# Performance work log

Hardware: AMD Instinct MI355X
Metric: run time of the kernel (lower is better)

## Reference

```python
import jax, jax.numpy as jnp
import numpy as np

C_M = 256
C = 32
N_HEAD = 8
EPS = 1e-5

def setup_inputs() -> dict:
    key = jax.random.key(0)
    ks = jax.random.split(key, 8)
    S, R = 512, 384  # N_seq, N_res
    msa = jax.random.normal(ks[0], (S, R, C_M), dtype=jnp.float32)
    init = lambda k, shape: 0.02 * jax.random.normal(k, shape, dtype=jnp.float32)
    return {
        "msa": msa,
        "ln_w": jnp.ones((N_HEAD, C_M), jnp.float32),
        "ln_b": jnp.zeros((N_HEAD, C_M), jnp.float32),
        "Wq": init(ks[1], (N_HEAD, C, C_M)),
        "Wk": init(ks[2], (N_HEAD, C, C_M)),
        "Wv": init(ks[3], (N_HEAD, C, C_M)),
        "Wg": init(ks[4], (N_HEAD, C, C_M)),
        "out_W": init(ks[5], (C_M, C * N_HEAD)),
        "out_b": jnp.zeros((C_M,), jnp.float32),
    }

def reference(msa, ln_w, ln_b, Wq, Wk, Wv, Wg, out_W, out_b):
    # msa: [s, r, c_m] -> x: [r, s, c_m]; attention over the sequence axis per column
    x = jnp.transpose(msa, (1, 0, 2))
    scale = 1.0 / np.sqrt(C)
    outs = []
    for h in range(N_HEAD):  # fixed small head loop (each head has its own LayerNorm)
        mu = jnp.mean(x, axis=-1, keepdims=True)
        var = jnp.mean((x - mu) ** 2, axis=-1, keepdims=True)
        p = (x - mu) * jax.lax.rsqrt(var + EPS) * ln_w[h] + ln_b[h]  # [r, s, c_m]
        q = jnp.einsum('rsm,cm->rsc', p, Wq[h])
        k = jnp.einsum('rsm,cm->rsc', p, Wk[h])
        v = jnp.einsum('rsm,cm->rsc', p, Wv[h])
        g = jax.nn.sigmoid(jnp.einsum('rsm,cm->rsc', p, Wg[h]))
        logits = scale * jnp.einsum('rsc,rtc->rst', q, k)  # [r, s, s]
        a = jax.nn.softmax(logits, axis=-2)  # faithful: softmax over dim=-2 as in source
        o = g * jnp.einsum('rst,rtc->rsc', a, v)  # gated per-head output
        outs.append(o)
    cat = jnp.concatenate(outs, axis=2)  # [r, s, c*N_head]
    out = jnp.einsum('rsd,md->rsm', cat, out_W) + out_b
    return jnp.transpose(out, (1, 0, 2))  # back to [s, r, c_m]
```

## Files before the change

### kernel.cpp

```cpp
#include <hip/hip_runtime.h>
#include <hip/hip_bf16.h>


#define S_DIM 512
#define R_DIM 384
#define CM    256
#define NH    8
#define NROWS (S_DIM*R_DIM)

typedef unsigned short u16;
typedef unsigned int   u32;
typedef short bf16x8 __attribute__((ext_vector_type(8)));
typedef float f32x4  __attribute__((ext_vector_type(4)));
typedef float f32x16 __attribute__((ext_vector_type(16)));
typedef int   v2i    __attribute__((ext_vector_type(2)));

#define MFMA16(a,b,c) __builtin_amdgcn_mfma_f32_16x16x32_bf16((a),(b),(c),0,0,0)
#define MFMA32(a,b,c) __builtin_amdgcn_mfma_f32_32x32x16_bf16((a),(b),(c),0,0,0)

__device__ __forceinline__ float lo16f(u32 u){ return __uint_as_float(u << 16); }
__device__ __forceinline__ float hi16f(u32 u){ return __uint_as_float(u & 0xffff0000u); }
__device__ __forceinline__ float b2f(u16 x){ return __uint_as_float(((u32)x) << 16); }
__device__ __forceinline__ u16 f2bf(float f){
  u32 u = __float_as_uint(f);
  return (u16)((u + 0x7fffu + ((u >> 16) & 1u)) >> 16);
}
__device__ __forceinline__ u32 pk2(float a, float b){
  return (u32)f2bf(a) | ((u32)f2bf(b) << 16);
}
__device__ __forceinline__ u32 cvtpk(float a, float b){
  u32 d;
  asm("v_cvt_pk_bf16_f32 %0, %1, %2" : "=v"(d) : "v"(a), "v"(b));
  return d;
}
__device__ __forceinline__ v2i pl32swap(u32 a, u32 b){
  return __builtin_amdgcn_permlane32_swap((int)a, (int)b, false, false);
}
__device__ __forceinline__ f32x16 zero16(){
  f32x16 z;
  #pragma unroll
  for(int q=0;q<16;q++) z[q]=0.f;
  return z;
}

#define SC2 0.2550348653f

__global__ void prep_w(const float* __restrict__ lnw, const float* __restrict__ lnb,
                       const float* __restrict__ Wq, const float* __restrict__ Wk,
                       const float* __restrict__ Wv, const float* __restrict__ Wg,
                       const float* __restrict__ oW,
                       float* __restrict__ ball, u16* __restrict__ Wfrag,
                       u16* __restrict__ oWhi, u16* __restrict__ oWlo){
  int blk = blockIdx.x, t = threadIdx.x;
  if (blk < 1024){
    int h = blk >> 7, row = blk & 127, mat = row >> 5, c = row & 31;
    const float* Ws = (mat==0?Wq: mat==1?Wk: mat==2?Wv:Wg) + (size_t)(h*32+c)*CM;
    float4 w4 = ((const float4*)Ws)[t];
    float4 l4 = ((const float4*)(lnw + (size_t)h*CM))[t];
    float4 b4 = ((const float4*)(lnb + (size_t)h*CM))[t];
    int kc = t >> 2, gg = (t >> 1) & 1, e0 = (t & 1) * 4;
    u16* dst = Wfrag + ((size_t)(((blk>>5)*16 + kc))*64 + gg*32 + c)*8 + e0;
    *(uint2*)dst = make_uint2(pk2(w4.x*l4.x, w4.y*l4.y), pk2(w4.z*l4.z, w4.w*l4.w));
    float p = w4.x*b4.x + w4.y*b4.y + w4.z*b4.z + w4.w*b4.w;
    #pragma unroll
    for(int off=32; off; off>>=1) p += __shfl_down(p, off);
    if(t==0) ball[blk] = p;
  } else {
    int m = blk - 1024;
    float4 w4 = ((const float4*)(oW + (size_t)m*CM))[t];
    u16 h0=f2bf(w4.x), h1=f2bf(w4.y), h2=f2bf(w4.z), h3=f2bf(w4.w);
    u16 l0=f2bf(w4.x-b2f(h0)), l1=f2bf(w4.y-b2f(h1));
    u16 l2=f2bf(w4.z-b2f(h2)), l3=f2bf(w4.w-b2f(h3));
    ((uint2*)(oWhi + (size_t)m*CM))[t] = make_uint2((u32)h0|((u32)h1<<16), (u32)h2|((u32)h3<<16));
    ((uint2*)(oWlo + (size_t)m*CM))[t] = make_uint2((u32)l0|((u32)l1<<16), (u32)l2|((u32)l3<<16));
  }
}

__global__ __launch_bounds__(256) void ln_xhat(const float* __restrict__ msa,
                                               u16* __restrict__ xhat){
  const int tid = threadIdx.x;
  const int n0 = blockIdx.x*64;
  const int i = tid >> 2, p = tid & 3;
  const int n = n0 + i, rr = n >> 9, s = n & 511;
  const float* src = msa + ((size_t)s*R_DIM + rr)*CM + p*64;
  float x[64]; float sum=0.f, sq=0.f;
  #pragma unroll
  for(int j=0;j<64;j+=4){
    float4 v = *(const float4*)(src + j);
    x[j]=v.x; x[j+1]=v.y; x[j+2]=v.z; x[j+3]=v.w;
    sum += v.x+v.y+v.z+v.w;
    sq  += v.x*v.x + v.y*v.y + v.z*v.z + v.w*v.w;
  }
  sum += __shfl_xor(sum,1); sum += __shfl_xor(sum,2);
  sq  += __shfl_xor(sq,1);  sq  += __shfl_xor(sq,2);
  float mu = sum*(1.f/256.f);
  float rs = rsqrtf(sq*(1.f/256.f) - mu*mu + 1e-5f);
  u16* dst = xhat + (size_t)n*CM + p*64;
  #pragma unroll
  for(int j=0;j<64;j+=2)
    *(u32*)(dst + j) = pk2((x[j]-mu)*rs, (x[j+1]-mu)*rs);
}

#define KF    0
#define VF    32768
#define DRED  65536
#define ATTN_LDS 81920

__global__ __launch_bounds__(512,2) void attn_fused4(const u16* __restrict__ xhat,
      const u16* __restrict__ Wfrag, const float* __restrict__ ball,
      u16* __restrict__ obuf){
  extern __shared__ char sm[];
  const int bid = blockIdx.x;
  const int xcd = bid & 7, kk2 = bid >> 3;
  const int r = xcd*48 + (kk2 >> 3);
  const int head = kk2 & 7;
  const int tid  = threadIdx.x;
  const int w    = tid >> 6;
  const int lane = tid & 63;
  const int gg = lane >> 5, j = lane & 31;
  const int n0 = r * 512;

  bf16x8 Qfr[2][2];

  {
    #pragma unroll
    for(int mat=0; mat<4; mat++){
      bf16x8 Wf[16];
      const u16* wsrc = Wfrag + ((size_t)((head*4+mat)*16)*64 + lane)*8;
      #pragma unroll
      for(int kc=0;kc<16;kc++) Wf[kc] = *(const bf16x8*)(wsrc + (size_t)kc*512);
      float bias16[16]; float biasv = 0.f;
      if (mat == 2) biasv = ball[head*128 + 64 + j];
      else {
        #pragma unroll
        for(int reg=0;reg<16;reg++)
          bias16[reg] = ball[head*128 + mat*32 + (reg&3) + 8*(reg>>2) + 4*gg];
      }
      #pragma unroll
      for(int st=0; st<2; st++){
        const int stg = 2*w + st;
        const u16* xr = xhat + ((size_t)(n0 + stg*32 + j))*CM + gg*8;
        f32x16 D = zero16();
        if (mat == 2){
          #pragma unroll
          for(int kc=0;kc<16;kc++) D = MFMA32(*(const bf16x8*)(xr + kc*16), Wf[kc], D);
        } else {
          #pragma unroll
          for(int kc=0;kc<16;kc++) D = MFMA32(Wf[kc], *(const bf16x8*)(xr + kc*16), D);
        }
        if (mat == 3){
          u32 gw[8];
          #pragma unroll
          for(int p=0;p<4;p++)
            #pragma unroll
            for(int hh=0;hh<2;hh++){
              float a = D[4*p+2*hh]   + bias16[4*p+2*hh];
              float b = D[4*p+2*hh+1] + bias16[4*p+2*hh+1];
              gw[p*2+hh] = cvtpk(1.f/(1.f + __expf(-a)), 1.f/(1.f + __expf(-b)));
            }
          int srow = n0 + stg*32 + j;
          u32* ob32 = (u32*)(obuf + (size_t)srow*CM + head*32);
          #pragma unroll
          for(int p=0;p<4;p++)
            #pragma unroll
            for(int hh=0;hh<2;hh++)
              ob32[4*p + 2*gg + hh] = gw[p*2+hh];
        } else {
          if (mat == 2){
            #pragma unroll
            for(int q=0;q<16;q++) D[q] += biasv;
          } else {
            #pragma unroll
            for(int q=0;q<16;q++) D[q] += bias16[q];
          }
          u32 Wd[8];
          #pragma unroll
          for(int p=0;p<4;p++)
            #pragma unroll
            for(int hh=0;hh<2;hh++)
              Wd[p*2+hh] = cvtpk(D[4*p+2*hh], D[4*p+2*hh+1]);
          u32 frag[2][4];
          #pragma unroll
          for(int T=0;T<2;T++)
            #pragma unroll
            for(int hh=0;hh<2;hh++){
              v2i res = pl32swap(Wd[4*T+hh], Wd[4*T+2+hh]);
              frag[T][hh] = (u32)res[0]; frag[T][2+hh] = (u32)res[1];
            }
          if (mat == 0){
            #pragma unroll
            for(int T=0;T<2;T++){
              union { u32 wu[4]; bf16x8 v; } u;
              u.wu[0]=frag[T][0]; u.wu[1]=frag[T][1]; u.wu[2]=frag[T][2]; u.wu[3]=frag[T][3];
              Qfr[st][T] = u.v;
            }
          } else {
            char* outbase = sm + (mat==1? KF : VF);
            #pragma unroll
            for(int T=0;T<2;T++)
              *(uint4*)(outbase + ((size_t)(stg*2+T)*64 + lane)*16) =
                  make_uint4(frag[T][0],frag[T][1],frag[T][2],frag[T][3]);
          }
        }
      }
    }
  }
  __syncthreads();

  {
    float* dred = (float*)(sm + DRED);
    for(int tt=0; tt<16; tt++){
      bf16x8 Kt0 = *(const bf16x8*)(sm + KF + ((size_t)(tt*2+0)*64 + lane)*16);
      bf16x8 Kt1 = *(const bf16x8*)(sm + KF + ((size_t)(tt*2+1)*64 + lane)*16);
      float dp = 0.f;
      #pragma unroll
      for(int sb=0; sb<2; sb++){
        f32x16 D1 = zero16();
        D1 = MFMA32(Qfr[sb][0], Kt0, D1);
        D1 = MFMA32(Qfr[sb][1], Kt1, D1);
        #pragma unroll
        for(int q=0;q<16;q++) dp += exp2f(D1[q]*SC2);
      }
      v2i rr = pl32swap(__float_as_uint(dp), __float_as_uint(dp));
      float tot = __uint_as_float((u32)rr[0]) + __uint_as_float((u32)rr[1]);
      if (lane < 32) dred[w*512 + tt*32 + j] = tot;
    }
  }
  __syncthreads();
  {
    float* dred = (float*)(sm + DRED);
    float s = 0.f;
    #pragma unroll
    for(int ww=0; ww<8; ww++) s += dred[ww*512 + tid];
    dred[tid] = 1.f / s;
  }
  __syncthreads();

  {
    const float* ivd = (const float*)(sm + DRED);
    #pragma unroll
    for(int it=0; it<4; it++){
      int ch = tid + it*512;
      int t0 = (ch>>7)*32 + ((ch>>6)&1)*16 + ((ch>>5)&1)*8;
      u32* pw = (u32*)(sm + VF + (size_t)ch*16);
      uint4 v = *(uint4*)pw;
      u32 wv[4] = {v.x, v.y, v.z, v.w};
      u32 nw[4];
      #pragma unroll
      for(int rr2=0;rr2<4;rr2++){
        float lo = lo16f(wv[rr2]) * ivd[t0 + 2*rr2];
        float hi = hi16f(wv[rr2]) * ivd[t0 + 2*rr2 + 1];
        nw[rr2] = cvtpk(lo, hi);
      }
      *(uint4*)pw = make_uint4(nw[0],nw[1],nw[2],nw[3]);
    }
  }
  __syncthreads();

  #pragma unroll
  for(int sb=0; sb<2; sb++){
    f32x16 O = zero16();
    for(int tt=0; tt<16; tt++){
      bf16x8 Kt0 = *(const bf16x8*)(sm + KF + ((size_t)(tt*2+0)*64 + lane)*16);
      bf16x8 Kt1 = *(const bf16x8*)(sm + KF + ((size_t)(tt*2+1)*64 + lane)*16);
      bf16x8 Vt0 = *(const bf16x8*)(sm + VF + ((size_t)(tt*2+0)*64 + lane)*16);
      bf16x8 Vt1 = *(const bf16x8*)(sm + VF + ((size_t)(tt*2+1)*64 + lane)*16);
      f32x16 D = zero16();
      D = MFMA32(Kt0, Qfr[sb][0], D);
      D = MFMA32(Kt1, Qfr[sb][1], D);
      u32 Wd[8];
      #pragma unroll
      for(int p=0;p<4;p++)
        #pragma unroll
        for(int hh=0;hh<2;hh++)
          Wd[p*2+hh] = cvtpk(exp2f(D[4*p+2*hh]*SC2), exp2f(D[4*p+2*hh+1]*SC2));
      union { u32 wu[4]; bf16x8 v; } pf0, pf1;
      #pragma unroll
      for(int hh=0;hh<2;hh++){
        v2i res = pl32swap(Wd[0+hh], Wd[2+hh]);
        pf0.wu[hh] = (u32)res[0]; pf0.wu[2+hh] = (u32)res[1];
        v2i res2 = pl32swap(Wd[4+hh], Wd[6+hh]);
        pf1.wu[hh] = (u32)res2[0]; pf1.wu[2+hh] = (u32)res2[1];
      }
      O = MFMA32(Vt0, pf0.v, O);
      O = MFMA32(Vt1, pf1.v, O);
    }
    const int stg = 2*w + sb;
    const int srow = n0 + stg*32 + j;
    u32* ob32 = (u32*)(obuf + (size_t)srow*CM + head*32);
    #pragma unroll
    for(int p=0;p<4;p++)
      #pragma unroll
      for(int hh=0;hh<2;hh++){
        u32 gv = ob32[4*p + 2*gg + hh];
        float o0 = O[4*p+2*hh]   * lo16f(gv);
        float o1 = O[4*p+2*hh+1] * hi16f(gv);
        ob32[4*p + 2*gg + hh] = cvtpk(o0, o1);
      }
  }
}

__global__ __launch_bounds__(256,2) void outproj(const u16* __restrict__ obuf,
      const u16* __restrict__ oWhi, const u16* __restrict__ oWlo,
      const float* __restrict__ ob, float* __restrict__ out){
  const int tid = threadIdx.x, w = tid>>6, lane = tid&63, g = lane>>4, i = lane&15;
  const int n0 = blockIdx.x*64 + w*16;
  const char* ab = (const char*)(obuf + (size_t)(n0 + i)*CM);
  const f32x4 zf = {0.f,0.f,0.f,0.f};
  f32x4 acc[16];
  #pragma unroll
  for(int ct=0;ct<16;ct++) acc[ct] = zf;
  #pragma unroll
  for(int kk=0; kk<8; kk++){
    bf16x8 a = *(const bf16x8*)(ab + kk*64 + g*16);
    #pragma unroll
    for(int ct=0; ct<16; ct++){
      const char* wh = (const char*)(oWhi + (size_t)(ct*16 + i)*CM);
      const char* wl = (const char*)(oWlo + (size_t)(ct*16 + i)*CM);
      bf16x8 bh = *(const bf16x8*)(wh + kk*64 + g*16);
      bf16x8 bl = *(const bf16x8*)(wl + kk*64 + g*16);
      acc[ct] = MFMA16(a, bh, acc[ct]);
      acc[ct] = MFMA16(a, bl, acc[ct]);
    }
  }
  #pragma unroll
  for(int ct=0; ct<16; ct++){
    float bias = ob[ct*16 + i];
    #pragma unroll
    for(int q=0; q<4; q++){
      int n = n0 + 4*g + q;
      out[((size_t)(n & 511)*R_DIM + (n >> 9))*CM + ct*16 + i] = acc[ct][q] + bias;
    }
  }
}

extern "C" void kernel_launch(void* const* d_in, const int* in_sizes, int n_in,
                              void* d_out, int out_size, void* d_ws, size_t ws_size,
                              hipStream_t stream){
  const float* msa = (const float*)d_in[0];
  const float* lnw = (const float*)d_in[1];
  const float* lnb = (const float*)d_in[2];
  const float* Wq  = (const float*)d_in[3];
  const float* Wk  = (const float*)d_in[4];
  const float* Wv  = (const float*)d_in[5];
  const float* Wg  = (const float*)d_in[6];
  const float* oW  = (const float*)d_in[7];
  const float* ob  = (const float*)d_in[8];
  float* out = (float*)d_out;

  char* ws = (char*)d_ws;
  u16*   Wfrag  = (u16*)(ws);
  float* ball   = (float*)(ws + 524288);
  u16*   oWhi   = (u16*)(ws + 528384);
  u16*   oWlo   = (u16*)(ws + 659456);
  u16*   xhat   = (u16*)(ws + 790528);
  u16*   obuf   = (u16*)(ws + 101453824);

  (void)hipFuncSetAttribute((const void*)attn_fused4,
                      hipFuncAttributeMaxDynamicSharedMemorySize, ATTN_LDS);

  prep_w<<<dim3(1280), dim3(64), 0, stream>>>(lnw, lnb, Wq, Wk, Wv, Wg, oW,
                                              ball, Wfrag, oWhi, oWlo);
  ln_xhat<<<dim3(NROWS/64), dim3(256), 0, stream>>>(msa, xhat);
  attn_fused4<<<dim3(R_DIM*NH), dim3(512), ATTN_LDS, stream>>>(xhat, Wfrag, ball, obuf);
  outproj<<<dim3(NROWS/64), dim3(256), 0, stream>>>(obuf, oWhi, oWlo, ob, out);
}
```

Baseline: 1.139 ms.

## Rewrite output projection with 32x32 MFMA and pre-fragmented weight layout

The output projection kernel now uses 32x32x16 MFMA tiles with 32 rows per wave and 128 rows per block, and loops over output column tiles instead of keeping all sixteen 16-wide accumulators live. prep_w writes the hi/lo bf16 weight splits in MFMA fragment order, so each lane reads its B operand contiguously. The aim is lower register pressure (launch bounds raised to 4 blocks), better weight-load coalescing and fewer MFMA issues. In exchange, the A rows are re-read from global memory for every column tile.

After: 1.039 ms. 8.8% less time.

```diff
diff --git a/kernel.cpp b/kernel.cpp
--- a/kernel.cpp
+++ b/kernel.cpp
@@ -15,7 +15,6 @@
 typedef float f32x16 __attribute__((ext_vector_type(16)));
 typedef int   v2i    __attribute__((ext_vector_type(2)));
 
-#define MFMA16(a,b,c) __builtin_amdgcn_mfma_f32_16x16x32_bf16((a),(b),(c),0,0,0)
 #define MFMA32(a,b,c) __builtin_amdgcn_mfma_f32_32x32x16_bf16((a),(b),(c),0,0,0)
 
 __device__ __forceinline__ float lo16f(u32 u){ return __uint_as_float(u << 16); }
@@ -50,15 +49,15 @@
                        const float* __restrict__ Wv, const float* __restrict__ Wg,
                        const float* __restrict__ oW,
                        float* __restrict__ ball, u16* __restrict__ Wfrag,
-                       u16* __restrict__ oWhi, u16* __restrict__ oWlo){
+                       u16* __restrict__ oWfh, u16* __restrict__ oWfl){
   int blk = blockIdx.x, t = threadIdx.x;
+  int kc = t >> 2, gg = (t >> 1) & 1, e0 = (t & 1) * 4;
   if (blk < 1024){
     int h = blk >> 7, row = blk & 127, mat = row >> 5, c = row & 31;
     const float* Ws = (mat==0?Wq: mat==1?Wk: mat==2?Wv:Wg) + (size_t)(h*32+c)*CM;
     float4 w4 = ((const float4*)Ws)[t];
     float4 l4 = ((const float4*)(lnw + (size_t)h*CM))[t];
     float4 b4 = ((const float4*)(lnb + (size_t)h*CM))[t];
-    int kc = t >> 2, gg = (t >> 1) & 1, e0 = (t & 1) * 4;
     u16* dst = Wfrag + ((size_t)(((blk>>5)*16 + kc))*64 + gg*32 + c)*8 + e0;
     *(uint2*)dst = make_uint2(pk2(w4.x*l4.x, w4.y*l4.y), pk2(w4.z*l4.z, w4.w*l4.w));
     float p = w4.x*b4.x + w4.y*b4.y + w4.z*b4.z + w4.w*b4.w;
@@ -71,8 +70,9 @@
     u16 h0=f2bf(w4.x), h1=f2bf(w4.y), h2=f2bf(w4.z), h3=f2bf(w4.w);
     u16 l0=f2bf(w4.x-b2f(h0)), l1=f2bf(w4.y-b2f(h1));
     u16 l2=f2bf(w4.z-b2f(h2)), l3=f2bf(w4.w-b2f(h3));
-    ((uint2*)(oWhi + (size_t)m*CM))[t] = make_uint2((u32)h0|((u32)h1<<16), (u32)h2|((u32)h3<<16));
-    ((uint2*)(oWlo + (size_t)m*CM))[t] = make_uint2((u32)l0|((u32)l1<<16), (u32)l2|((u32)l3<<16));
+    size_t idx = ((size_t)(((m>>5)*16 + kc))*64 + gg*32 + (m&31))*8 + e0;
+    *(uint2*)(oWfh + idx) = make_uint2((u32)h0|((u32)h1<<16), (u32)h2|((u32)h3<<16));
+    *(uint2*)(oWfl + idx) = make_uint2((u32)l0|((u32)l1<<16), (u32)l2|((u32)l3<<16));
   }
 }
 
@@ -300,36 +300,29 @@
   }
 }
 
-__global__ __launch_bounds__(256,2) void outproj(const u16* __restrict__ obuf,
-      const u16* __restrict__ oWhi, const u16* __restrict__ oWlo,
+__global__ __launch_bounds__(256,4) void outproj2(const u16* __restrict__ obuf,
+      const u16* __restrict__ oWfh, const u16* __restrict__ oWfl,
       const float* __restrict__ ob, float* __restrict__ out){
-  const int tid = threadIdx.x, w = tid>>6, lane = tid&63, g = lane>>4, i = lane&15;
-  const int n0 = blockIdx.x*64 + w*16;
-  const char* ab = (const char*)(obuf + (size_t)(n0 + i)*CM);
-  const f32x4 zf = {0.f,0.f,0.f,0.f};
-  f32x4 acc[16];
-  #pragma unroll
-  for(int ct=0;ct<16;ct++) acc[ct] = zf;
-  #pragma unroll
-  for(int kk=0; kk<8; kk++){
-    bf16x8 a = *(const bf16x8*)(ab + kk*64 + g*16);
-    #pragma unroll
-    for(int ct=0; ct<16; ct++){
-      const char* wh = (const char*)(oWhi + (size_t)(ct*16 + i)*CM);
-      const char* wl = (const char*)(oWlo + (size_t)(ct*16 + i)*CM);
-      bf16x8 bh = *(const bf16x8*)(wh + kk*64 + g*16);
-      bf16x8 bl = *(const bf16x8*)(wl + kk*64 + g*16);
-      acc[ct] = MFMA16(a, bh, acc[ct]);
-      acc[ct] = MFMA16(a, bl, acc[ct]);
-    }
-  }
-  #pragma unroll
-  for(int ct=0; ct<16; ct++){
-    float bias = ob[ct*16 + i];
-    #pragma unroll
-    for(int q=0; q<4; q++){
-      int n = n0 + 4*g + q;
-      out[((size_t)(n & 511)*R_DIM + (n >> 9))*CM + ct*16 + i] = acc[ct][q] + bias;
+  const int tid = threadIdx.x, w = tid>>6, lane = tid&63;
+  const int gg = lane>>5, j = lane&31;
+  const int row0 = blockIdx.x*128 + w*32;
+  const u16* arow = obuf + (size_t)(row0 + j)*CM + gg*8;
+  #pragma unroll 2
+  for(int ct=0; ct<8; ct++){
+    f32x16 acc = zero16();
+    const u16* bh = oWfh + ((size_t)(ct*16)*64 + lane)*8;
+    const u16* bl = oWfl + ((size_t)(ct*16)*64 + lane)*8;
+    #pragma unroll
+    for(int kc=0; kc<16; kc++){
+      bf16x8 a = *(const bf16x8*)(arow + kc*16);
+      acc = MFMA32(a, *(const bf16x8*)(bh + (size_t)kc*512), acc);
+      acc = MFMA32(a, *(const bf16x8*)(bl + (size_t)kc*512), acc);
+    }
+    float bias = ob[ct*32 + j];
+    #pragma unroll
+    for(int reg=0; reg<16; reg++){
+      int n = row0 + (reg&3) + 8*(reg>>2) + 4*gg;
+      out[((size_t)(n & 511)*R_DIM + (n >> 9))*CM + ct*32 + j] = acc[reg] + bias;
     }
   }
 }
@@ -351,8 +344,8 @@
   char* ws = (char*)d_ws;
   u16*   Wfrag  = (u16*)(ws);
   float* ball   = (float*)(ws + 524288);
-  u16*   oWhi   = (u16*)(ws + 528384);
-  u16*   oWlo   = (u16*)(ws + 659456);
+  u16*   oWfh   = (u16*)(ws + 528384);
+  u16*   oWfl   = (u16*)(ws + 659456);
   u16*   xhat   = (u16*)(ws + 790528);
   u16*   obuf   = (u16*)(ws + 101453824);
 
@@ -360,8 +353,8 @@
                       hipFuncAttributeMaxDynamicSharedMemorySize, ATTN_LDS);
 
   prep_w<<<dim3(1280), dim3(64), 0, stream>>>(lnw, lnb, Wq, Wk, Wv, Wg, oW,
-                                              ball, Wfrag, oWhi, oWlo);
+                                              ball, Wfrag, oWfh, oWfl);
   ln_xhat<<<dim3(NROWS/64), dim3(256), 0, stream>>>(msa, xhat);
   attn_fused4<<<dim3(R_DIM*NH), dim3(512), ATTN_LDS, stream>>>(xhat, Wfrag, ball, obuf);
-  outproj<<<dim3(NROWS/64), dim3(256), 0, stream>>>(obuf, oWhi, oWlo, ob, out);
-}
+  outproj2<<<dim3(NROWS/128), dim3(256), 0, stream>>>(obuf, oWfh, oWfl, ob, out);
+}
```
